# Performance work log

Measured on AMD Instinct MI355X. Metric: run time of the kernel, lower is better.

The kernel has to match this reference:

```python
import jax, jax.numpy as jnp
import numpy as np

B, S, D, H = 2, 2048, 1024, 16
HD = D // H  # head_dim = 64


def setup_inputs() -> dict:
    key = jax.random.key(0)
    ks = jax.random.split(key, 6)
    sc = 0.02
    return {
        "x": jax.random.normal(ks[0], (B, S, D), dtype=jnp.float32),
        "W_query": jax.random.normal(ks[1], (D, D), dtype=jnp.float32) * sc,
        "W_key": jax.random.normal(ks[2], (D, D), dtype=jnp.float32) * sc,
        "W_value": jax.random.normal(ks[3], (D, D), dtype=jnp.float32) * sc,
        "W_out": jax.random.normal(ks[4], (D, D), dtype=jnp.float32) * sc,
        "b_out": jnp.zeros((D,), dtype=jnp.float32),
    }


def reference(x, W_query, W_key, W_value, W_out, b_out):
    b, s, _ = x.shape
    # torch nn.Linear: y = x @ W.T ; split into heads [b, h, s, hd]
    def proj(W):
        return (x @ W.T).reshape(b, s, H, HD).transpose(0, 2, 1, 3)

    q, k, v = proj(W_query), proj(W_key), proj(W_value)
    scores = jnp.einsum("bhqd,bhkd->bhqk", q, k)  # [b, h, s, s]
    causal = jnp.tril(jnp.ones((s, s), dtype=bool))  # True = keep
    scores = jnp.where(causal, scores, -jnp.inf)
    weights = jax.nn.softmax(scores / np.sqrt(HD).astype(np.float32), axis=-1)
    # dropout p=0.0 -> identity
    ctx = jnp.einsum("bhqk,bhkd->bhqd", weights, v)
    ctx = ctx.transpose(0, 2, 1, 3).reshape(b, s, D)
    return ctx @ W_out.T + b_out
```

## Files before the change

kernel.cpp:

```cpp
#include <hip/hip_runtime.h>
#include <stdint.h>

#define B_  2
#define S_  2048
#define D_  1024
#define H_  16
#define HD_ 64
#define M_  (B_*S_)

typedef __attribute__((ext_vector_type(8)))  short bf16x8;
typedef __attribute__((ext_vector_type(4)))  float f32x4;
typedef __attribute__((ext_vector_type(16))) float f32x16;
typedef __attribute__((ext_vector_type(4)))  unsigned int u32x4;


__device__ __forceinline__ unsigned short f2bf(float f) {
    unsigned int u = __float_as_uint(f);
    unsigned int r = (u + 0x7fffu + ((u >> 16) & 1u)) >> 16;
    return (unsigned short)r;
}

__device__ __forceinline__ unsigned int cvt_pk_bf16(float lo, float hi) {
    unsigned int r;
    asm("v_cvt_pk_bf16_f32 %0, %1, %2" : "=v"(r) : "v"(lo), "v"(hi));
    return r;
}

__device__ __forceinline__ void gload_lds16(const void* g, void* l) {
    __builtin_amdgcn_global_load_lds(
        (const __attribute__((address_space(1))) unsigned int*)g,
        (__attribute__((address_space(3))) unsigned int*)l,
        16, 0, 0);
}


__global__ __launch_bounds__(256) void cast_all(
    const float* __restrict__ x,
    const float* __restrict__ wq, const float* __restrict__ wk,
    const float* __restrict__ wv, const float* __restrict__ wo,
    unsigned short* __restrict__ dst)
{
    int b = blockIdx.x;
    const float* src;
    size_t soff, doff;
    float sc = 1.0f;
    if (b < 2048) {
        src = x; soff = (size_t)b * 2048; doff = soff;
    } else {
        int r  = (b - 2048) >> 9;
        int lb = (b - 2048) & 511;
        src = (r == 0) ? wq : (r == 1) ? wk : (r == 2) ? wv : wo;
        if (r <= 1) sc = 0.4246609093670877f;
        soff = (size_t)lb * 2048;
        doff = (size_t)4194304 + (size_t)r * 1048576 + soff;
    }
    int idx = threadIdx.x * 8;
    float4 a = *reinterpret_cast<const float4*>(src + soff + idx);
    float4 c = *reinterpret_cast<const float4*>(src + soff + idx + 4);
    unsigned short t[8];
    t[0]=f2bf(a.x*sc); t[1]=f2bf(a.y*sc); t[2]=f2bf(a.z*sc); t[3]=f2bf(a.w*sc);
    t[4]=f2bf(c.x*sc); t[5]=f2bf(c.y*sc); t[6]=f2bf(c.z*sc); t[7]=f2bf(c.w*sc);
    *reinterpret_cast<uint4*>(dst + doff + idx) = *reinterpret_cast<const uint4*>(t);
}


template <bool BIAS, typename CT>
__global__ __launch_bounds__(256) void gemm_bt(
    const unsigned short* __restrict__ A,
    const unsigned short* __restrict__ Bm,
    CT* __restrict__ C,
    const float* __restrict__ bias,
    int M, int N, int K)
{
    constexpr int BK = 32;
    __shared__ unsigned short As[128 * BK];
    __shared__ unsigned short Bs[128 * BK];

    const int tid  = threadIdx.x;
    const int lane = tid & 63;
    const int wid  = tid >> 6;
    const int wr = wid >> 1, wc = wid & 1;
    const int l15 = lane & 15, lhi = lane >> 4;
    const int tm = blockIdx.y * 128, tn = blockIdx.x * 128;

    f32x4 acc[4][4] = {};

    const int srow = (lane >> 2);
    const int scol = (lane & 3) * 8;

    for (int k0 = 0; k0 < K; k0 += BK) {
        __syncthreads();
        #pragma unroll
        for (int i = 0; i < 2; ++i) {
            int chunk = wid * 2 + i;
            int row = chunk * 16 + srow;
            gload_lds16(A  + (size_t)(tm + row) * K + k0 + scol, (void*)(As + chunk * 512));
            gload_lds16(Bm + (size_t)(tn + row) * K + k0 + scol, (void*)(Bs + chunk * 512));
        }
        __syncthreads();

        bf16x8 af[4], bfr[4];
        #pragma unroll
        for (int i = 0; i < 4; ++i)
            af[i] = *reinterpret_cast<const bf16x8*>(As + (wr * 64 + i * 16 + l15) * BK + lhi * 8);
        #pragma unroll
        for (int j = 0; j < 4; ++j)
            bfr[j] = *reinterpret_cast<const bf16x8*>(Bs + (wc * 64 + j * 16 + l15) * BK + lhi * 8);
        #pragma unroll
        for (int i = 0; i < 4; ++i)
            #pragma unroll
            for (int j = 0; j < 4; ++j)
                acc[i][j] = __builtin_amdgcn_mfma_f32_16x16x32_bf16(af[i], bfr[j], acc[i][j], 0, 0, 0);
    }

    #pragma unroll
    for (int i = 0; i < 4; ++i) {
        #pragma unroll
        for (int j = 0; j < 4; ++j) {
            int col = tn + wc * 64 + j * 16 + l15;
            float bv = BIAS ? bias[col] : 0.0f;
            #pragma unroll
            for (int r = 0; r < 4; ++r) {
                int row = tm + wr * 64 + i * 16 + lhi * 4 + r;
                float v = acc[i][j][r] + bv;
                if constexpr (sizeof(CT) == 2) {
                    ((unsigned short*)C)[(size_t)row * N + col] = f2bf(v);
                } else {
                    ((float*)C)[(size_t)row * N + col] = v;
                }
            }
        }
    }
}


__global__ __launch_bounds__(256) void gemm_qkv(
    const unsigned short* __restrict__ A,
    const unsigned short* __restrict__ Bm,
    unsigned short* __restrict__ Cqk,
    unsigned short* __restrict__ Vt)
{
    constexpr int BK = 32, K = 1024;
    __shared__ unsigned short As[128 * BK];
    __shared__ unsigned short Bs[128 * BK];

    const int tid  = threadIdx.x;
    const int lane = tid & 63;
    const int wid  = tid >> 6;
    const int wr = wid >> 1, wc = wid & 1;
    const int l15 = lane & 15, lhi = lane >> 4;
    const int tm = blockIdx.y * 128, tn = blockIdx.x * 128;

    f32x4 acc[4][4] = {};

    const int srow = (lane >> 2);
    const int scol = (lane & 3) * 8;

    for (int k0 = 0; k0 < K; k0 += BK) {
        __syncthreads();
        #pragma unroll
        for (int i = 0; i < 2; ++i) {
            int chunk = wid * 2 + i;
            int row = chunk * 16 + srow;
            gload_lds16(A  + (size_t)(tm + row) * K + k0 + scol, (void*)(As + chunk * 512));
            gload_lds16(Bm + (size_t)(tn + row) * K + k0 + scol, (void*)(Bs + chunk * 512));
        }
        __syncthreads();

        bf16x8 af[4], bfr[4];
        #pragma unroll
        for (int i = 0; i < 4; ++i)
            af[i] = *reinterpret_cast<const bf16x8*>(As + (wr * 64 + i * 16 + l15) * BK + lhi * 8);
        #pragma unroll
        for (int j = 0; j < 4; ++j)
            bfr[j] = *reinterpret_cast<const bf16x8*>(Bs + (wc * 64 + j * 16 + l15) * BK + lhi * 8);
        #pragma unroll
        for (int i = 0; i < 4; ++i)
            #pragma unroll
            for (int j = 0; j < 4; ++j)
                acc[i][j] = __builtin_amdgcn_mfma_f32_16x16x32_bf16(af[i], bfr[j], acc[i][j], 0, 0, 0);
    }

    const bool isV = (tn >= 2048);
    #pragma unroll
    for (int i = 0; i < 4; ++i) {
        #pragma unroll
        for (int j = 0; j < 4; ++j) {
            int col = tn + wc * 64 + j * 16 + l15;
            int row0 = tm + wr * 64 + i * 16 + lhi * 4;
            if (!isV) {
                #pragma unroll
                for (int r = 0; r < 4; ++r)
                    Cqk[(size_t)(row0 + r) * 2048 + col] = f2bf(acc[i][j][r]);
            } else {
                unsigned short t[4];
                #pragma unroll
                for (int r = 0; r < 4; ++r) t[r] = f2bf(acc[i][j][r]);
                *reinterpret_cast<uint2*>(Vt + (size_t)(col - 2048) * M_ + row0) =
                    *reinterpret_cast<const uint2*>(t);
            }
        }
    }
}


__global__ __launch_bounds__(256) void attn_kernel(
    const unsigned short* __restrict__ QK,
    const unsigned short* __restrict__ VT,
    unsigned short* __restrict__ Ctx)
{
    __shared__ unsigned short Ks[4][2][32 * 64];
    __shared__ unsigned short Vs[4][2][64 * 32];

    const int tid  = threadIdx.x;
    const int lane = tid & 63;
    const int wid  = tid >> 6;
    const int l31  = lane & 31;
    const int hi   = lane >> 5;

    const int lin  = blockIdx.x;
    const int xcd  = lin & 7;
    const int idx  = lin >> 3;
    const int bh   = xcd + 8 * (idx & 3);
    const int qb   = 63 - (idx >> 2);
    const int b = bh >> 4, h = bh & 15;
    const size_t baseRow = (size_t)b * S_;
    const int qw = qb * 32;
    const int q  = qw + l31;

    bf16x8 qf[4];
    #pragma unroll
    for (int s = 0; s < 4; ++s)
        qf[s] = *reinterpret_cast<const bf16x8*>(
            QK + (baseRow + q) * 2048 + h * HD_ + s * 16 + hi * 8);

    float l = 0.0f;
    f32x16 oacc[2] = {};

    const int nkt = qb + 1;

    const int kr  = lane >> 3;
    const int ks  = lane & 7;
    const int vr  = lane >> 2;
    const int vsl = lane & 3;

#define STAGE(kt_, bi_) do {                                                   \
    int k0_ = (kt_) * 32;                                                      \
    _Pragma("unroll")                                                          \
    for (int i_ = 0; i_ < 4; ++i_) {                                           \
        int krow_ = i_ * 8 + kr;                                               \
        int ksc_  = (ks ^ kr) * 8;                                             \
        gload_lds16(QK + (baseRow + k0_ + krow_) * 2048 + D_ + h * HD_ + ksc_, \
                    (void*)(&Ks[wid][bi_][i_ * 512]));                         \
        int vrow_ = i_ * 16 + vr;                                              \
        int vsc_  = (vsl ^ ((vrow_ >> 1) & 3)) * 8;                            \
        gload_lds16(VT + (size_t)(h * HD_ + vrow_) * M_ + baseRow + k0_ + vsc_,\
                    (void*)(&Vs[wid][bi_][i_ * 512]));                         \
    } } while (0)

    if (wid < nkt) {
        STAGE(wid, 0);
        int cur = 0;
        for (int kt = wid; kt < nkt; kt += 4) {
            if (kt + 4 < nkt) {
                STAGE(kt + 4, cur ^ 1);
                asm volatile("s_waitcnt vmcnt(8)" ::: "memory");
            } else {
                asm volatile("s_waitcnt vmcnt(0)" ::: "memory");
            }
            __builtin_amdgcn_sched_barrier(0);

            const unsigned short* Kc = &Ks[wid][cur][0];
            const unsigned short* Vc = &Vs[wid][cur][0];

            bf16x8 vf[2][2];
            #pragma unroll
            for (int dt = 0; dt < 2; ++dt)
                #pragma unroll
                for (int s = 0; s < 2; ++s) {
                    int d = dt * 32 + l31;
                    int sl = (2 * s + hi) ^ ((d >> 1) & 3);
                    vf[dt][s] = *reinterpret_cast<const bf16x8*>(Vc + d * 32 + sl * 8);
                }

            f32x16 sc = {};
            #pragma unroll
            for (int s = 0; s < 4; ++s) {
                int sl = (2 * s + hi) ^ (l31 & 7);
                bf16x8 kf = *reinterpret_cast<const bf16x8*>(Kc + l31 * 64 + sl * 8);
                sc = __builtin_amdgcn_mfma_f32_32x32x16_bf16(kf, qf[s], sc, 0, 0, 0);
            }

            if (kt == qb) {
                #pragma unroll
                for (int r = 0; r < 16; ++r) {
                    int kl = kt * 32 + (r & 3) + 8 * (r >> 2) + 4 * hi;
                    if (kl > q) sc[r] = -INFINITY;
                }
            }

            unsigned int g0, g1, g2, g3, g4, g5, g6, g7;
            float ps = 0.0f;
            {
                float e0, e1, e2, e3;
                e0=exp2f(sc[0]);  e1=exp2f(sc[1]);  e2=exp2f(sc[2]);  e3=exp2f(sc[3]);
                ps += (e0+e1)+(e2+e3); g0 = cvt_pk_bf16(e0,e1); g1 = cvt_pk_bf16(e2,e3);
                e0=exp2f(sc[4]);  e1=exp2f(sc[5]);  e2=exp2f(sc[6]);  e3=exp2f(sc[7]);
                ps += (e0+e1)+(e2+e3); g2 = cvt_pk_bf16(e0,e1); g3 = cvt_pk_bf16(e2,e3);
                e0=exp2f(sc[8]);  e1=exp2f(sc[9]);  e2=exp2f(sc[10]); e3=exp2f(sc[11]);
                ps += (e0+e1)+(e2+e3); g4 = cvt_pk_bf16(e0,e1); g5 = cvt_pk_bf16(e2,e3);
                e0=exp2f(sc[12]); e1=exp2f(sc[13]); e2=exp2f(sc[14]); e3=exp2f(sc[15]);
                ps += (e0+e1)+(e2+e3); g6 = cvt_pk_bf16(e0,e1); g7 = cvt_pk_bf16(e2,e3);
            }
            l += ps;

            asm("v_permlane32_swap_b32 %0, %1" : "+v"(g0), "+v"(g2));
            asm("v_permlane32_swap_b32 %0, %1" : "+v"(g1), "+v"(g3));
            asm("v_permlane32_swap_b32 %0, %1" : "+v"(g4), "+v"(g6));
            asm("v_permlane32_swap_b32 %0, %1" : "+v"(g5), "+v"(g7));
            bf16x8 pa0 = __builtin_bit_cast(bf16x8, (u32x4){g0, g1, g2, g3});
            bf16x8 pa1 = __builtin_bit_cast(bf16x8, (u32x4){g4, g5, g6, g7});

            __builtin_amdgcn_s_setprio(1);
            #pragma unroll
            for (int dt = 0; dt < 2; ++dt) {
                oacc[dt] = __builtin_amdgcn_mfma_f32_32x32x16_bf16(pa0, vf[dt][0], oacc[dt], 0, 0, 0);
                oacc[dt] = __builtin_amdgcn_mfma_f32_32x32x16_bf16(pa1, vf[dt][1], oacc[dt], 0, 0, 0);
            }
            __builtin_amdgcn_s_setprio(0);

            cur ^= 1;
        }
    }
#undef STAGE

    float* Olw = (float*)&Ks[wid][0][0];
    float* Lpw = (float*)&Vs[wid][0][0];
    #pragma unroll
    for (int r = 0; r < 16; ++r) {
        int qr = (r & 3) + 8 * (r >> 2) + 4 * hi;
        Olw[qr * 64 + l31]      = oacc[0][r];
        Olw[qr * 64 + 32 + l31] = oacc[1][r];
    }
    float lc = l + __shfl_xor(l, 32, 64);
    if (hi == 0) Lpw[l31] = lc;
    __syncthreads();

    const int cq = tid >> 3;
    const int cd = (tid & 7) * 8;
    float s[8] = {};
    float lt = 0.0f;
    #pragma unroll
    for (int w = 0; w < 4; ++w) {
        const float* O = (const float*)&Ks[w][0][0];
        const f32x4 a = *reinterpret_cast<const f32x4*>(O + cq * 64 + cd);
        const f32x4 c = *reinterpret_cast<const f32x4*>(O + cq * 64 + cd + 4);
        s[0]+=a[0]; s[1]+=a[1]; s[2]+=a[2]; s[3]+=a[3];
        s[4]+=c[0]; s[5]+=c[1]; s[6]+=c[2]; s[7]+=c[3];
        lt += ((const float*)&Vs[w][0][0])[cq];
    }
    float inv = 1.0f / lt;
    unsigned short o[8];
    #pragma unroll
    for (int e = 0; e < 8; ++e) o[e] = f2bf(s[e] * inv);
    *reinterpret_cast<uint4*>(Ctx + (baseRow + qw + cq) * D_ + h * HD_ + cd) =
        *reinterpret_cast<const uint4*>(o);
}


extern "C" void kernel_launch(void* const* d_in, const int* in_sizes, int n_in,
                              void* d_out, int out_size, void* d_ws, size_t ws_size,
                              hipStream_t stream) {
    const float* x  = (const float*)d_in[0];
    const float* wq = (const float*)d_in[1];
    const float* wk = (const float*)d_in[2];
    const float* wv = (const float*)d_in[3];
    const float* wo = (const float*)d_in[4];
    const float* bo = (const float*)d_in[5];

    unsigned short* ws = (unsigned short*)d_ws;
    unsigned short* xb  = ws;
    unsigned short* wqb = xb  + 4194304;
    unsigned short* wob = wqb + 3145728;
    unsigned short* QKb = wob + 1048576;
    unsigned short* VT  = QKb + 8388608;
    unsigned short* Cx  = VT  + 4194304;

    cast_all<<<4096, 256, 0, stream>>>(x, wq, wk, wv, wo, xb);

    gemm_qkv<<<dim3(24, 32), 256, 0, stream>>>(xb, wqb, QKb, VT);

    attn_kernel<<<2048, 256, 0, stream>>>(QKb, VT, Cx);

    gemm_bt<true, float><<<dim3(8, 32), 256, 0, stream>>>(
        Cx, wob, (float*)d_out, bo, M_, D_, D_);
}
```

Measured before the change: 119.2 us.

## Share K/V tiles across four waves each owning a separate query block

The attention kernel previously assigned one 32-row query block per workgroup and split the key range across four waves, combining the partial outputs through LDS at the end. Now each workgroup handles 128 query rows, one 32-row block per wave. All waves cooperatively stage a shared K/V tile each iteration with a barrier, and each wave writes its own normalized output directly, so no cross-wave reduction is needed. This cuts redundant K/V global loads and the LDS reduction. In exchange it adds per-tile barriers, leaves waves idle on causal tiles past their diagonal, launches only 512 workgroups, and writes output as scattered 2-byte stores.

```diff
diff --git a/kernel.cpp b/kernel.cpp
--- a/kernel.cpp
+++ b/kernel.cpp
@@ -209,8 +209,8 @@
     const unsigned short* __restrict__ VT,
     unsigned short* __restrict__ Ctx)
 {
-    __shared__ unsigned short Ks[4][2][32 * 64];
-    __shared__ unsigned short Vs[4][2][64 * 32];
+    __shared__ unsigned short Ks[2][32 * 64];
+    __shared__ unsigned short Vs[2][64 * 32];
 
     const int tid  = threadIdx.x;
     const int lane = tid & 63;
@@ -222,11 +222,13 @@
     const int xcd  = lin & 7;
     const int idx  = lin >> 3;
     const int bh   = xcd + 8 * (idx & 3);
-    const int qb   = 63 - (idx >> 2);
+    const int qsb  = 15 - (idx >> 2);
     const int b = bh >> 4, h = bh & 15;
     const size_t baseRow = (size_t)b * S_;
-    const int qw = qb * 32;
+    const int qw = qsb * 128 + wid * 32;
     const int q  = qw + l31;
+    const int myKT = qw >> 5;
+    const int nkt  = qsb * 4 + 4;
 
     bf16x8 qf[4];
     #pragma unroll
@@ -237,134 +239,106 @@
     float l = 0.0f;
     f32x16 oacc[2] = {};
 
-    const int nkt = qb + 1;
-
-    const int kr  = lane >> 3;
-    const int ks  = lane & 7;
-    const int vr  = lane >> 2;
-    const int vsl = lane & 3;
+    const int kr8  = lane >> 3;
+    const int ksl  = lane & 7;
+    const int vr16 = lane >> 2;
+    const int vsl  = lane & 3;
 
 #define STAGE(kt_, bi_) do {                                                   \
     int k0_ = (kt_) * 32;                                                      \
-    _Pragma("unroll")                                                          \
-    for (int i_ = 0; i_ < 4; ++i_) {                                           \
-        int krow_ = i_ * 8 + kr;                                               \
-        int ksc_  = (ks ^ kr) * 8;                                             \
-        gload_lds16(QK + (baseRow + k0_ + krow_) * 2048 + D_ + h * HD_ + ksc_, \
-                    (void*)(&Ks[wid][bi_][i_ * 512]));                         \
-        int vrow_ = i_ * 16 + vr;                                              \
-        int vsc_  = (vsl ^ ((vrow_ >> 1) & 3)) * 8;                            \
-        gload_lds16(VT + (size_t)(h * HD_ + vrow_) * M_ + baseRow + k0_ + vsc_,\
-                    (void*)(&Vs[wid][bi_][i_ * 512]));                         \
-    } } while (0)
-
-    if (wid < nkt) {
-        STAGE(wid, 0);
-        int cur = 0;
-        for (int kt = wid; kt < nkt; kt += 4) {
-            if (kt + 4 < nkt) {
-                STAGE(kt + 4, cur ^ 1);
-                asm volatile("s_waitcnt vmcnt(8)" ::: "memory");
-            } else {
-                asm volatile("s_waitcnt vmcnt(0)" ::: "memory");
+    int krow_ = wid * 8 + kr8;                                                 \
+    int ksc_  = (ksl ^ kr8) * 8;                                               \
+    gload_lds16(QK + (baseRow + k0_ + krow_) * 2048 + D_ + h * HD_ + ksc_,     \
+                (void*)(&Ks[bi_][wid * 512]));                                 \
+    int vrow_ = wid * 16 + vr16;                                               \
+    int vsc_  = (vsl ^ ((vr16 >> 1) & 3)) * 8;                                 \
+    gload_lds16(VT + (size_t)(h * HD_ + vrow_) * M_ + baseRow + k0_ + vsc_,    \
+                (void*)(&Vs[bi_][wid * 512]));                                 \
+    } while (0)
+
+    STAGE(0, 0);
+
+    for (int kt = 0; kt < nkt; ++kt) {
+        const int cur = kt & 1;
+        asm volatile("s_waitcnt vmcnt(0)" ::: "memory");
+        __builtin_amdgcn_s_barrier();
+        __builtin_amdgcn_sched_barrier(0);
+        if (kt + 1 < nkt) STAGE(kt + 1, cur ^ 1);
+
+        if (kt > myKT) continue;
+
+        const unsigned short* Kc = &Ks[cur][0];
+        const unsigned short* Vc = &Vs[cur][0];
+
+        bf16x8 vf[2][2];
+        #pragma unroll
+        for (int dt = 0; dt < 2; ++dt)
+            #pragma unroll
+            for (int s = 0; s < 2; ++s) {
+                int d = dt * 32 + l31;
+                int sl = (2 * s + hi) ^ ((d >> 1) & 3);
+                vf[dt][s] = *reinterpret_cast<const bf16x8*>(Vc + d * 32 + sl * 8);
             }
-            __builtin_amdgcn_sched_barrier(0);
-
-            const unsigned short* Kc = &Ks[wid][cur][0];
-            const unsigned short* Vc = &Vs[wid][cur][0];
-
-            bf16x8 vf[2][2];
-            #pragma unroll
-            for (int dt = 0; dt < 2; ++dt)
-                #pragma unroll
-                for (int s = 0; s < 2; ++s) {
-                    int d = dt * 32 + l31;
-                    int sl = (2 * s + hi) ^ ((d >> 1) & 3);
-                    vf[dt][s] = *reinterpret_cast<const bf16x8*>(Vc + d * 32 + sl * 8);
-                }
-
-            f32x16 sc = {};
-            #pragma unroll
-            for (int s = 0; s < 4; ++s) {
-                int sl = (2 * s + hi) ^ (l31 & 7);
-                bf16x8 kf = *reinterpret_cast<const bf16x8*>(Kc + l31 * 64 + sl * 8);
-                sc = __builtin_amdgcn_mfma_f32_32x32x16_bf16(kf, qf[s], sc, 0, 0, 0);
+
+        f32x16 sc = {};
+        #pragma unroll
+        for (int s = 0; s < 4; ++s) {
+            int sl = (2 * s + hi) ^ (l31 & 7);
+            bf16x8 kf = *reinterpret_cast<const bf16x8*>(Kc + l31 * 64 + sl * 8);
+            sc = __builtin_amdgcn_mfma_f32_32x32x16_bf16(kf, qf[s], sc, 0, 0, 0);
+        }
+
+        if (kt == myKT) {
+            #pragma unroll
+            for (int r = 0; r < 16; ++r) {
+                int kl = kt * 32 + (r & 3) + 8 * (r >> 2) + 4 * hi;
+                if (kl > q) sc[r] = -INFINITY;
             }
-
-            if (kt == qb) {
-                #pragma unroll
-                for (int r = 0; r < 16; ++r) {
-                    int kl = kt * 32 + (r & 3) + 8 * (r >> 2) + 4 * hi;
-                    if (kl > q) sc[r] = -INFINITY;
-                }
-            }
-
-            unsigned int g0, g1, g2, g3, g4, g5, g6, g7;
-            float ps = 0.0f;
-            {
-                float e0, e1, e2, e3;
-                e0=exp2f(sc[0]);  e1=exp2f(sc[1]);  e2=exp2f(sc[2]);  e3=exp2f(sc[3]);
-                ps += (e0+e1)+(e2+e3); g0 = cvt_pk_bf16(e0,e1); g1 = cvt_pk_bf16(e2,e3);
-                e0=exp2f(sc[4]);  e1=exp2f(sc[5]);  e2=exp2f(sc[6]);  e3=exp2f(sc[7]);
-                ps += (e0+e1)+(e2+e3); g2 = cvt_pk_bf16(e0,e1); g3 = cvt_pk_bf16(e2,e3);
-                e0=exp2f(sc[8]);  e1=exp2f(sc[9]);  e2=exp2f(sc[10]); e3=exp2f(sc[11]);
-                ps += (e0+e1)+(e2+e3); g4 = cvt_pk_bf16(e0,e1); g5 = cvt_pk_bf16(e2,e3);
-                e0=exp2f(sc[12]); e1=exp2f(sc[13]); e2=exp2f(sc[14]); e3=exp2f(sc[15]);
-                ps += (e0+e1)+(e2+e3); g6 = cvt_pk_bf16(e0,e1); g7 = cvt_pk_bf16(e2,e3);
-            }
-            l += ps;
-
-            asm("v_permlane32_swap_b32 %0, %1" : "+v"(g0), "+v"(g2));
-            asm("v_permlane32_swap_b32 %0, %1" : "+v"(g1), "+v"(g3));
-            asm("v_permlane32_swap_b32 %0, %1" : "+v"(g4), "+v"(g6));
-            asm("v_permlane32_swap_b32 %0, %1" : "+v"(g5), "+v"(g7));
-            bf16x8 pa0 = __builtin_bit_cast(bf16x8, (u32x4){g0, g1, g2, g3});
-            bf16x8 pa1 = __builtin_bit_cast(bf16x8, (u32x4){g4, g5, g6, g7});
-
-            __builtin_amdgcn_s_setprio(1);
-            #pragma unroll
-            for (int dt = 0; dt < 2; ++dt) {
-                oacc[dt] = __builtin_amdgcn_mfma_f32_32x32x16_bf16(pa0, vf[dt][0], oacc[dt], 0, 0, 0);
-                oacc[dt] = __builtin_amdgcn_mfma_f32_32x32x16_bf16(pa1, vf[dt][1], oacc[dt], 0, 0, 0);
-            }
-            __builtin_amdgcn_s_setprio(0);
-
-            cur ^= 1;
-        }
+        }
+
+        unsigned int g0, g1, g2, g3, g4, g5, g6, g7;
+        float ps = 0.0f;
+        {
+            float e0, e1, e2, e3;
+            e0=exp2f(sc[0]);  e1=exp2f(sc[1]);  e2=exp2f(sc[2]);  e3=exp2f(sc[3]);
+            ps += (e0+e1)+(e2+e3); g0 = cvt_pk_bf16(e0,e1); g1 = cvt_pk_bf16(e2,e3);
+            e0=exp2f(sc[4]);  e1=exp2f(sc[5]);  e2=exp2f(sc[6]);  e3=exp2f(sc[7]);
+            ps += (e0+e1)+(e2+e3); g2 = cvt_pk_bf16(e0,e1); g3 = cvt_pk_bf16(e2,e3);
+            e0=exp2f(sc[8]);  e1=exp2f(sc[9]);  e2=exp2f(sc[10]); e3=exp2f(sc[11]);
+            ps += (e0+e1)+(e2+e3); g4 = cvt_pk_bf16(e0,e1); g5 = cvt_pk_bf16(e2,e3);
+            e0=exp2f(sc[12]); e1=exp2f(sc[13]); e2=exp2f(sc[14]); e3=exp2f(sc[15]);
+            ps += (e0+e1)+(e2+e3); g6 = cvt_pk_bf16(e0,e1); g7 = cvt_pk_bf16(e2,e3);
+        }
+        l += ps;
+
+        asm("v_permlane32_swap_b32 %0, %1" : "+v"(g0), "+v"(g2));
+        asm("v_permlane32_swap_b32 %0, %1" : "+v"(g1), "+v"(g3));
+        asm("v_permlane32_swap_b32 %0, %1" : "+v"(g4), "+v"(g6));
+        asm("v_permlane32_swap_b32 %0, %1" : "+v"(g5), "+v"(g7));
+        bf16x8 pa0 = __builtin_bit_cast(bf16x8, (u32x4){g0, g1, g2, g3});
+        bf16x8 pa1 = __builtin_bit_cast(bf16x8, (u32x4){g4, g5, g6, g7});
+
+        __builtin_amdgcn_s_setprio(1);
+        #pragma unroll
+        for (int dt = 0; dt < 2; ++dt) {
+            oacc[dt] = __builtin_amdgcn_mfma_f32_32x32x16_bf16(pa0, vf[dt][0], oacc[dt], 0, 0, 0);
+            oacc[dt] = __builtin_amdgcn_mfma_f32_32x32x16_bf16(pa1, vf[dt][1], oacc[dt], 0, 0, 0);
+        }
+        __builtin_amdgcn_s_setprio(0);
     }
 #undef STAGE
 
-    float* Olw = (float*)&Ks[wid][0][0];
-    float* Lpw = (float*)&Vs[wid][0][0];
+    l += __shfl_xor(l, 32, 64);
+    float inv = 1.0f / l;
     #pragma unroll
     for (int r = 0; r < 16; ++r) {
         int qr = (r & 3) + 8 * (r >> 2) + 4 * hi;
-        Olw[qr * 64 + l31]      = oacc[0][r];
-        Olw[qr * 64 + 32 + l31] = oacc[1][r];
-    }
-    float lc = l + __shfl_xor(l, 32, 64);
-    if (hi == 0) Lpw[l31] = lc;
-    __syncthreads();
-
-    const int cq = tid >> 3;
-    const int cd = (tid & 7) * 8;
-    float s[8] = {};
-    float lt = 0.0f;
-    #pragma unroll
-    for (int w = 0; w < 4; ++w) {
-        const float* O = (const float*)&Ks[w][0][0];
-        const f32x4 a = *reinterpret_cast<const f32x4*>(O + cq * 64 + cd);
-        const f32x4 c = *reinterpret_cast<const f32x4*>(O + cq * 64 + cd + 4);
-        s[0]+=a[0]; s[1]+=a[1]; s[2]+=a[2]; s[3]+=a[3];
-        s[4]+=c[0]; s[5]+=c[1]; s[6]+=c[2]; s[7]+=c[3];
-        lt += ((const float*)&Vs[w][0][0])[cq];
-    }
-    float inv = 1.0f / lt;
-    unsigned short o[8];
-    #pragma unroll
-    for (int e = 0; e < 8; ++e) o[e] = f2bf(s[e] * inv);
-    *reinterpret_cast<uint4*>(Ctx + (baseRow + qw + cq) * D_ + h * HD_ + cd) =
-        *reinterpret_cast<const uint4*>(o);
+        float ir = __shfl(inv, qr, 32);
+        #pragma unroll
+        for (int dt = 0; dt < 2; ++dt)
+            Ctx[(baseRow + qw + qr) * D_ + h * HD_ + dt * 32 + l31] =
+                f2bf(oacc[dt][r] * ir);
+    }
 }
 
 
@@ -390,7 +364,7 @@
 
     gemm_qkv<<<dim3(24, 32), 256, 0, stream>>>(xb, wqb, QKb, VT);
 
-    attn_kernel<<<2048, 256, 0, stream>>>(QKb, VT, Cx);
+    attn_kernel<<<512, 256, 0, stream>>>(QKb, VT, Cx);
 
     gemm_bt<true, float><<<dim3(8, 32), 256, 0, stream>>>(
         Cx, wob, (float*)d_out, bo, M_, D_, D_);
```

Result: slower. 141.4 us (+18.6%).

## Drop K/V double buffering to halve LDS and raise attention occupancy

Applied to the files above, without the earlier changes.

Removes the per-wave double-buffered K/V staging and instead loads each tile synchronously inside the loop, splitting the waits so the QK^T MFMAs can begin once K arrives while V is still in flight. This halves LDS use, and together with launch_bounds(256,5) aims for more resident blocks per CU, so other waves can hide load latency. The cross-wave output reduction is split into two 32-column phases so it fits the smaller LDS buffers. The cost is the loss of explicit prefetch within a wave, plus extra barriers in the epilogue.

```diff
diff --git a/kernel.cpp b/kernel.cpp
--- a/kernel.cpp
+++ b/kernel.cpp
@@ -204,13 +204,13 @@
 }
 
 
-__global__ __launch_bounds__(256) void attn_kernel(
+__global__ __launch_bounds__(256, 5) void attn_kernel(
     const unsigned short* __restrict__ QK,
     const unsigned short* __restrict__ VT,
     unsigned short* __restrict__ Ctx)
 {
-    __shared__ unsigned short Ks[4][2][32 * 64];
-    __shared__ unsigned short Vs[4][2][64 * 32];
+    __shared__ unsigned short Ks[4][32 * 64];
+    __shared__ unsigned short Vs[4][64 * 32];
 
     const int tid  = threadIdx.x;
     const int lane = tid & 63;
@@ -219,9 +219,8 @@
     const int hi   = lane >> 5;
 
     const int lin  = blockIdx.x;
-    const int xcd  = lin & 7;
     const int idx  = lin >> 3;
-    const int bh   = xcd + 8 * (idx & 3);
+    const int bh   = (lin & 7) + 8 * (idx & 3);
     const int qb   = 63 - (idx >> 2);
     const int b = bh >> 4, h = bh & 15;
     const size_t baseRow = (size_t)b * S_;
@@ -244,44 +243,33 @@
     const int vr  = lane >> 2;
     const int vsl = lane & 3;
 
-#define STAGE(kt_, bi_) do {                                                   \
+#define STAGE_K(kt_) do {                                                      \
     int k0_ = (kt_) * 32;                                                      \
     _Pragma("unroll")                                                          \
     for (int i_ = 0; i_ < 4; ++i_) {                                           \
         int krow_ = i_ * 8 + kr;                                               \
         int ksc_  = (ks ^ kr) * 8;                                             \
         gload_lds16(QK + (baseRow + k0_ + krow_) * 2048 + D_ + h * HD_ + ksc_, \
-                    (void*)(&Ks[wid][bi_][i_ * 512]));                         \
+                    (void*)(&Ks[wid][i_ * 512]));                              \
+    } } while (0)
+#define STAGE_V(kt_) do {                                                      \
+    int k0_ = (kt_) * 32;                                                      \
+    _Pragma("unroll")                                                          \
+    for (int i_ = 0; i_ < 4; ++i_) {                                           \
         int vrow_ = i_ * 16 + vr;                                              \
         int vsc_  = (vsl ^ ((vrow_ >> 1) & 3)) * 8;                            \
         gload_lds16(VT + (size_t)(h * HD_ + vrow_) * M_ + baseRow + k0_ + vsc_,\
-                    (void*)(&Vs[wid][bi_][i_ * 512]));                         \
+                    (void*)(&Vs[wid][i_ * 512]));                              \
     } } while (0)
 
     if (wid < nkt) {
-        STAGE(wid, 0);
-        int cur = 0;
         for (int kt = wid; kt < nkt; kt += 4) {
-            if (kt + 4 < nkt) {
-                STAGE(kt + 4, cur ^ 1);
-                asm volatile("s_waitcnt vmcnt(8)" ::: "memory");
-            } else {
-                asm volatile("s_waitcnt vmcnt(0)" ::: "memory");
-            }
+            STAGE_K(kt);
+            STAGE_V(kt);
+            asm volatile("s_waitcnt vmcnt(4)" ::: "memory");
             __builtin_amdgcn_sched_barrier(0);
 
-            const unsigned short* Kc = &Ks[wid][cur][0];
-            const unsigned short* Vc = &Vs[wid][cur][0];
-
-            bf16x8 vf[2][2];
-            #pragma unroll
-            for (int dt = 0; dt < 2; ++dt)
-                #pragma unroll
-                for (int s = 0; s < 2; ++s) {
-                    int d = dt * 32 + l31;
-                    int sl = (2 * s + hi) ^ ((d >> 1) & 3);
-                    vf[dt][s] = *reinterpret_cast<const bf16x8*>(Vc + d * 32 + sl * 8);
-                }
+            const unsigned short* Kc = &Ks[wid][0];
 
             f32x16 sc = {};
             #pragma unroll
@@ -321,6 +309,20 @@
             bf16x8 pa0 = __builtin_bit_cast(bf16x8, (u32x4){g0, g1, g2, g3});
             bf16x8 pa1 = __builtin_bit_cast(bf16x8, (u32x4){g4, g5, g6, g7});
 
+            asm volatile("s_waitcnt vmcnt(0)" ::: "memory");
+            __builtin_amdgcn_sched_barrier(0);
+
+            const unsigned short* Vc = &Vs[wid][0];
+            bf16x8 vf[2][2];
+            #pragma unroll
+            for (int dt = 0; dt < 2; ++dt)
+                #pragma unroll
+                for (int s = 0; s < 2; ++s) {
+                    int d = dt * 32 + l31;
+                    int sl = (2 * s + hi) ^ ((d >> 1) & 3);
+                    vf[dt][s] = *reinterpret_cast<const bf16x8*>(Vc + d * 32 + sl * 8);
+                }
+
             __builtin_amdgcn_s_setprio(1);
             #pragma unroll
             for (int dt = 0; dt < 2; ++dt) {
@@ -328,43 +330,44 @@
                 oacc[dt] = __builtin_amdgcn_mfma_f32_32x32x16_bf16(pa1, vf[dt][1], oacc[dt], 0, 0, 0);
             }
             __builtin_amdgcn_s_setprio(0);
-
-            cur ^= 1;
-        }
-    }
-#undef STAGE
-
-    float* Olw = (float*)&Ks[wid][0][0];
-    float* Lpw = (float*)&Vs[wid][0][0];
-    #pragma unroll
-    for (int r = 0; r < 16; ++r) {
-        int qr = (r & 3) + 8 * (r >> 2) + 4 * hi;
-        Olw[qr * 64 + l31]      = oacc[0][r];
-        Olw[qr * 64 + 32 + l31] = oacc[1][r];
-    }
+        }
+    }
+#undef STAGE_K
+#undef STAGE_V
+
+    float* Olw = (float*)&Ks[wid][0];
+    float* Lpw = (float*)&Vs[wid][0];
     float lc = l + __shfl_xor(l, 32, 64);
     if (hi == 0) Lpw[l31] = lc;
-    __syncthreads();
 
     const int cq = tid >> 3;
-    const int cd = (tid & 7) * 8;
-    float s[8] = {};
-    float lt = 0.0f;
+    const int cd = (tid & 7) * 4;
+    float inv = 0.0f;
     #pragma unroll
-    for (int w = 0; w < 4; ++w) {
-        const float* O = (const float*)&Ks[w][0][0];
-        const f32x4 a = *reinterpret_cast<const f32x4*>(O + cq * 64 + cd);
-        const f32x4 c = *reinterpret_cast<const f32x4*>(O + cq * 64 + cd + 4);
-        s[0]+=a[0]; s[1]+=a[1]; s[2]+=a[2]; s[3]+=a[3];
-        s[4]+=c[0]; s[5]+=c[1]; s[6]+=c[2]; s[7]+=c[3];
-        lt += ((const float*)&Vs[w][0][0])[cq];
-    }
-    float inv = 1.0f / lt;
-    unsigned short o[8];
-    #pragma unroll
-    for (int e = 0; e < 8; ++e) o[e] = f2bf(s[e] * inv);
-    *reinterpret_cast<uint4*>(Ctx + (baseRow + qw + cq) * D_ + h * HD_ + cd) =
-        *reinterpret_cast<const uint4*>(o);
+    for (int ph = 0; ph < 2; ++ph) {
+        __syncthreads();
+        #pragma unroll
+        for (int r = 0; r < 16; ++r) {
+            int qr = (r & 3) + 8 * (r >> 2) + 4 * hi;
+            Olw[qr * 32 + l31] = oacc[ph][r];
+        }
+        __syncthreads();
+        float s0 = 0, s1 = 0, s2 = 0, s3 = 0, lt = 0;
+        #pragma unroll
+        for (int w = 0; w < 4; ++w) {
+            const float* O = (const float*)&Ks[w][0];
+            f32x4 a = *reinterpret_cast<const f32x4*>(O + cq * 32 + cd);
+            s0 += a[0]; s1 += a[1]; s2 += a[2]; s3 += a[3];
+            if (ph == 0) lt += ((const float*)&Vs[w][0])[cq];
+        }
+        if (ph == 0) inv = 1.0f / lt;
+        unsigned short o[4];
+        o[0] = f2bf(s0 * inv); o[1] = f2bf(s1 * inv);
+        o[2] = f2bf(s2 * inv); o[3] = f2bf(s3 * inv);
+        *reinterpret_cast<uint2*>(
+            Ctx + (baseRow + qw + cq) * D_ + h * HD_ + ph * 32 + cd) =
+            *reinterpret_cast<const uint2*>(o);
+    }
 }
 
 
```

Measured after the change: 139.7 us. 1.17x slower.
